# Kernel optimization log

Hardware: AMD Instinct MI355X
Metric: run time of the kernel (lower is better)

## Reference

```python
import jax, jax.numpy as jnp
import numpy as np

EPS = float(np.finfo(np.float32).eps)
H = 256          # hidden_size
K = 10           # num_event_types
B, S = 32, 4096  # batch, seq_len


def _linear_params(kw, kb, fan_in, fan_out):
    # torch nn.Linear default init (uniform +-1/sqrt(fan_in)), then abs + clamp(min=eps)
    bound = 1.0 / np.sqrt(fan_in)
    w = jnp.clip(jnp.abs(jax.random.uniform(kw, (fan_out, fan_in), minval=-bound, maxval=bound, dtype=jnp.float32)), EPS)
    b = jnp.clip(jnp.abs(jax.random.uniform(kb, (fan_out,), minval=-bound, maxval=bound, dtype=jnp.float32)), EPS)
    return w, b


def setup_inputs() -> dict:
    key = jax.random.key(0)
    ks = jax.random.split(key, 12)
    w1, b1 = _linear_params(ks[0], ks[1], 1, H)        # layer_dense_1
    w2, b2 = _linear_params(ks[2], ks[3], 2 * H, H)    # layer_dense_2
    wA, bA = _linear_params(ks[4], ks[5], H, H)        # module_list[0]
    wB, bB = _linear_params(ks[6], ks[7], H, H)        # module_list[1]
    w3, b3 = _linear_params(ks[8], ks[9], H, K)        # layer_dense_3 linear
    hidden_states = jax.random.normal(ks[10], (B, S, H), dtype=jnp.float32)
    time_delta_seqs = jax.random.uniform(ks[11], (B, S), dtype=jnp.float32)
    return dict(hidden_states=hidden_states, time_delta_seqs=time_delta_seqs,
                w1=w1, b1=b1, w2=w2, b2=b2, wA=wA, bA=bA, wB=wB, bB=bB, w3=w3, b3=b3)


def _cumul_hazard(td, h, w1, b1, w2, b2, wA, bA, wB, bB, w3, b3):
    # layer_dense_1: Linear(1 -> H) on td[..., None]
    t = td[..., None] * w1[:, 0] + b1                      # [B,S,H]
    out = jnp.tanh(jnp.concatenate([h, t], axis=-1) @ w2.T + b2)  # [B,S,H]
    out = jnp.tanh(out @ wA.T + bA)
    out = jnp.tanh(out @ wB.T + bB)
    return jax.nn.softplus(out @ w3.T + b3)                # [B,S,K]


def reference(hidden_states, time_delta_seqs, w1, b1, w2, b2, wA, bA, wB, bB, w3, b3):
    f = lambda td: _cumul_hazard(td, hidden_states, w1, b1, w2, b2, wA, bA, wB, bB, w3, b3)
    # Each output element depends only on its own t[b,s] (elementwise in time),
    # so a single forward-mode JVP with tangent=ones yields the exact per-element
    # derivative for ALL event types at once (fuses torch's per-type grad loop).
    integral_lambda, d_dt = jax.jvp(f, (time_delta_seqs,), (jnp.ones_like(time_delta_seqs),))
    # torch takes grad of .mean() over [B,S], which scales the derivative by 1/(B*S)
    derivative_integral_lambda = d_dt / time_delta_seqs.size
    return integral_lambda, derivative_integral_lambda
```

## Files before the change

### kernel.cpp

```cpp
#include <hip/hip_runtime.h>
#include <hip/hip_bf16.h>
#include <stdint.h>

typedef __bf16 bf16x8 __attribute__((ext_vector_type(8)));
typedef __bf16 bf16x4 __attribute__((ext_vector_type(4)));
typedef float  f32x4  __attribute__((ext_vector_type(4)));
typedef float  f32x2  __attribute__((ext_vector_type(2)));

#define MFMA16(a,b,c) __builtin_amdgcn_mfma_f32_16x16x32_bf16((a),(b),(c),0,0,0)

static constexpr int H_   = 256;
static constexpr int KEV  = 10;
static constexpr int NTOK = 32 * 4096;

__device__ __forceinline__ float ptanh(float x){
    float t = x * x;
    float n = fmaf(t, t + 105.0f, 945.0f);
    float d = fmaf(t, fmaf(t, 15.0f, 420.0f), 945.0f);
    float r = x * n * __builtin_amdgcn_rcpf(d);
    return __builtin_amdgcn_fmed3f(r, -1.0f, 1.0f);
}

__device__ __forceinline__ bf16x8 cvtFrag(const float* p){
    f32x4 a = *(const f32x4*)p;
    f32x4 b = *(const f32x4*)(p + 4);
    bf16x8 r;
    #pragma unroll
    for (int j = 0; j < 4; ++j){ r[j] = (__bf16)a[j]; r[4 + j] = (__bf16)b[j]; }
    return r;
}

__global__ void prep_vc(const float* __restrict__ w1, const float* __restrict__ b1,
                        const float* __restrict__ w2, const float* __restrict__ b2,
                        const float* __restrict__ b3, float* __restrict__ vc){
    int j = blockIdx.x * 4 + (threadIdx.x >> 6);
    int l = threadIdx.x & 63;
    const float* row = w2 + (size_t)j * (2 * H_) + H_;
    float v = 0.f, cc = 0.f;
    #pragma unroll
    for (int i = 0; i < 4; ++i){
        int k = l + 64 * i;
        float w = row[k];
        v  += w * w1[k];
        cc += w * b1[k];
    }
    #pragma unroll
    for (int off = 32; off; off >>= 1){
        v  += __shfl_down(v,  off, 64);
        cc += __shfl_down(cc, off, 64);
    }
    if (l == 0){ vc[j] = v; vc[H_ + j] = cc + b2[j]; }
    if (blockIdx.x == 0 && threadIdx.x < 16)
        vc[2 * H_ + threadIdx.x] = (threadIdx.x < KEV) ? b3[threadIdx.x] : 0.0f;
}

__global__ void prep_pack(const float* __restrict__ w2, const float* __restrict__ wA,
                          const float* __restrict__ wB, const float* __restrict__ w3,
                          __hip_bfloat16* __restrict__ pk){
    int b  = blockIdx.x;
    int L  = b >> 4, n0 = b & 15;
    const float* W; int K, nrows;
    if (b == 48){ W = w3; K = H_; nrows = KEV; }
    else { W = (L == 0) ? w2 : ((L == 1) ? wA : wB); K = (L == 0) ? 2 * H_ : H_; nrows = 16; }
    __hip_bfloat16* dst = pk + (size_t)b * 4096;
    int t = threadIdx.x;
    #pragma unroll
    for (int u = 0; u < 2; ++u){
        int slot = t * 2 + u;
        int s = slot >> 6, q = (slot >> 4) & 3, c = slot & 15;
        int rr = (b == 48) ? c : (n0 * 16 + c);
        if (c < nrows){
            const float* src = W + (size_t)rr * K + 32 * s + 8 * q;
            #pragma unroll
            for (int j = 0; j < 8; ++j) dst[slot * 8 + j] = __float2bfloat16(src[j]);
        } else {
            #pragma unroll
            for (int j = 0; j < 8; ++j) dst[slot * 8 + j] = __float2bfloat16(0.0f);
        }
    }
}

typedef const __attribute__((address_space(1))) void* gvp;
typedef __attribute__((address_space(3)))       void* lvp;

__device__ __forceinline__ void stage_chunk(const __hip_bfloat16* wpk, __hip_bfloat16* buf,
                                            int g, int wave, int lane){
    const char* src = (const char*)wpk + (size_t)g * 8192 + wave * 2048 + lane * 16;
    char*       dst = (char*)buf + wave * 2048;
    __builtin_amdgcn_global_load_lds((gvp)(const void*)src,          (lvp)(void*)dst,          16, 0, 0);
    __builtin_amdgcn_global_load_lds((gvp)(const void*)(src + 1024), (lvp)(void*)(dst + 1024), 16, 0, 0);
}

__global__ __launch_bounds__(256, 3) void chfn_kernel(
    const float* __restrict__ hs, const float* __restrict__ td,
    const __hip_bfloat16* __restrict__ wpk,
    const float* __restrict__ bA, const float* __restrict__ bB,
    const float* __restrict__ vc,
    float* __restrict__ out)
{
    __shared__ __hip_bfloat16 sW[2 * 4096];
    __shared__ __hip_bfloat16 sA[4 * 16 * H_];
    __shared__ __hip_bfloat16 sT[4 * 512];

    const int tid  = threadIdx.x;
    const int wave = tid >> 6;
    const int lane = tid & 63;
    const int q    = lane >> 4;
    const int c    = lane & 15;
    const int tb   = blockIdx.x * 64 + wave * 16;
    const int wrow = wave * 16;
    const int xr   = (c >> 1) & 7;
    const int sx   = (c >> 1) & 1;
    const int ws   = q * 16 + c;
    const int e0w  = wave * 512 + 32 * c + 4 * q;
    const int r0w  = wave * 512 + 32 * c + ((8 * q) ^ (sx << 4));

    stage_chunk(wpk, sW, 0, wave, lane);

    bf16x8 aF[8], TA[8], TB[8];
    {
        const float* h0 = hs + (size_t)(tb + c) * H_ + 8 * q;
        #pragma unroll
        for (int s = 0; s < 8; ++s) aF[s] = cvtFrag(h0 + 32 * s);
    }
    float myTd = td[tb + c];

    #pragma unroll
    for (int jj = 0; jj < 8; ++jj){
        #pragma unroll
        for (int t = 0; t < 2; ++t){
            int n0 = 2 * jj + t;
            __syncthreads();
            stage_chunk(wpk, sW + ((n0 + 1) & 1) * 4096, n0 + 1, wave, lane);
            bf16x8 W[8];
            {   const bf16x8* b = (const bf16x8*)(sW + (n0 & 1) * 4096) + ws;
                #pragma unroll
                for (int s = 0; s < 8; ++s) W[s] = b[s * 64];
            }
            f32x4 v4 = *(const f32x4*)(vc + n0 * 16 + 4 * q);
            f32x4 c4 = *(const f32x4*)(vc + H_ + n0 * 16 + 4 * q);
            f32x4 fa = c4;
            f32x4 fb = {0.f,0.f,0.f,0.f};
            #pragma unroll
            for (int s = 0; s < 4; ++s){
                fa = MFMA16(W[s],     aF[s],     fa);
                fb = MFMA16(W[s + 4], aF[s + 4], fb);
            }
            bf16x4 pa, pd;
            #pragma unroll
            for (int r = 0; r < 4; ++r){
                float x  = fmaf(myTd, v4[r], fa[r] + fb[r]);
                float th = ptanh(x);
                float dd = fmaf(-th, th, 1.0f) * v4[r];
                pa[r] = (__bf16)th; pd[r] = (__bf16)dd;
            }
            int chn = 2 * n0 + (q >> 1);
            int off = (wrow + c) * H_ + ((((chn + 4 * c) & 31) ^ xr) << 3) + ((q & 1) << 2);
            *(bf16x4*)((void*)(sA + off)) = pa;
            *(bf16x4*)((void*)(sT + e0w + ((t ^ sx) << 4))) = pd;
        }
        TB[jj] = *(const bf16x8*)(sT + r0w);
    }

    auto run_layer = [&](const float* __restrict__ bias, int g0,
                         bf16x8 (&Tin)[8], bf16x8 (&Tout)[8]){
        {
            const __hip_bfloat16* a0 = sA + (wrow + c) * H_;
            #pragma unroll
            for (int s = 0; s < 8; ++s){
                int g8 = ((((4 * s + q) + 4 * c) & 31) ^ xr) << 3;
                aF[s] = *(const bf16x8*)(a0 + g8);
            }
        }
        #pragma unroll
        for (int jj = 0; jj < 8; ++jj){
            #pragma unroll
            for (int t = 0; t < 2; ++t){
                int n0 = 2 * jj + t;
                int g  = g0 + n0;
                __syncthreads();
                stage_chunk(wpk, sW + ((g + 1) & 1) * 4096, g + 1, wave, lane);
                bf16x8 W[8];
                {   const bf16x8* b = (const bf16x8*)(sW + (g & 1) * 4096) + ws;
                    #pragma unroll
                    for (int s = 0; s < 8; ++s) W[s] = b[s * 64];
                }
                f32x4 b4 = *(const f32x4*)(bias + n0 * 16 + 4 * q);
                f32x4 fa = b4;
                f32x4 fb = {0.f,0.f,0.f,0.f};
                f32x4 ga = {0.f,0.f,0.f,0.f};
                f32x4 gb = {0.f,0.f,0.f,0.f};
                #pragma unroll
                for (int s = 0; s < 4; ++s){
                    fa = MFMA16(W[s],     aF[s],      fa);
                    ga = MFMA16(W[s],     Tin[s],     ga);
                    fb = MFMA16(W[s + 4], aF[s + 4],  fb);
                    gb = MFMA16(W[s + 4], Tin[s + 4], gb);
                }
                bf16x4 pa, pd;
                #pragma unroll
                for (int r = 0; r < 4; ++r){
                    float th = ptanh(fa[r] + fb[r]);
                    float dd = fmaf(-th, th, 1.0f) * (ga[r] + gb[r]);
                    pa[r] = (__bf16)th; pd[r] = (__bf16)dd;
                }
                int chn = 2 * n0 + (q >> 1);
                int off = (wrow + c) * H_ + ((((chn + 4 * c) & 31) ^ xr) << 3) + ((q & 1) << 2);
                *(bf16x4*)((void*)(sA + off)) = pa;
                *(bf16x4*)((void*)(sT + e0w + ((t ^ sx) << 4))) = pd;
            }
            Tout[jj] = *(const bf16x8*)(sT + r0w);
        }
    };

    run_layer(bA, 16, TB, TA);
    run_layer(bB, 32, TA, TB);

    {
        __syncthreads();
        bf16x8 W[8];
        {   const bf16x8* b = (const bf16x8*)sW + ws;
            #pragma unroll
            for (int s = 0; s < 8; ++s) W[s] = b[s * 64];
        }
        const __hip_bfloat16* a0 = sA + (wrow + c) * H_;
        #pragma unroll
        for (int s = 0; s < 8; ++s){
            int g8 = ((((4 * s + q) + 4 * c) & 31) ^ xr) << 3;
            aF[s] = *(const bf16x8*)(a0 + g8);
        }
        f32x4 b4 = *(const f32x4*)(vc + 2 * H_ + 4 * q);
        f32x4 fa = b4;
        f32x4 fb = {0.f,0.f,0.f,0.f};
        f32x4 ga = {0.f,0.f,0.f,0.f};
        f32x4 gb = {0.f,0.f,0.f,0.f};
        #pragma unroll
        for (int s = 0; s < 4; ++s){
            fa = MFMA16(W[s],     aF[s],     fa);
            ga = MFMA16(W[s],     TB[s],     ga);
            fb = MFMA16(W[s + 4], aF[s + 4], fb);
            gb = MFMA16(W[s + 4], TB[s + 4], gb);
        }
        int fbase = 4 * q;
        size_t token = tb + c;
        float sp[4], dv[4];
        #pragma unroll
        for (int r = 0; r < 4; ++r){
            float z  = fa[r] + fb[r];
            float a  = fabsf(z);
            float e  = __builtin_amdgcn_exp2f(-1.4426950408889634f * a);
            sp[r] = fmaxf(z, 0.f) + 0.69314718055994531f * __builtin_amdgcn_logf(1.0f + e);
            float sg = __builtin_amdgcn_rcpf(1.0f + e);
            sg = (z >= 0.f) ? sg : 1.0f - sg;
            dv[r] = sg * (ga[r] + gb[r]) * (1.0f / 131072.0f);
        }
        float* o0 = out + token * KEV + fbase;
        float* o1 = out + (size_t)NTOK * KEV + token * KEV + fbase;
        if (q < 2){
            *(f32x2*)o0       = (f32x2){sp[0], sp[1]};
            *(f32x2*)(o0 + 2) = (f32x2){sp[2], sp[3]};
            *(f32x2*)o1       = (f32x2){dv[0], dv[1]};
            *(f32x2*)(o1 + 2) = (f32x2){dv[2], dv[3]};
        } else if (q == 2){
            *(f32x2*)o0 = (f32x2){sp[0], sp[1]};
            *(f32x2*)o1 = (f32x2){dv[0], dv[1]};
        }
    }
}

extern "C" void kernel_launch(void* const* d_in, const int* in_sizes, int n_in,
                              void* d_out, int out_size, void* d_ws, size_t ws_size,
                              hipStream_t stream){
    const float* hs = (const float*)d_in[0];
    const float* td = (const float*)d_in[1];
    const float* w1 = (const float*)d_in[2];
    const float* b1 = (const float*)d_in[3];
    const float* w2 = (const float*)d_in[4];
    const float* b2 = (const float*)d_in[5];
    const float* wA = (const float*)d_in[6];
    const float* bA = (const float*)d_in[7];
    const float* wB = (const float*)d_in[8];
    const float* bB = (const float*)d_in[9];
    const float* w3 = (const float*)d_in[10];
    const float* b3 = (const float*)d_in[11];

    float*          vc  = (float*)d_ws;
    __hip_bfloat16* wpk = (__hip_bfloat16*)((char*)d_ws + 4096);
    float*          outp = (float*)d_out;

    prep_vc  <<<64, 256, 0, stream>>>(w1, b1, w2, b2, b3, vc);
    prep_pack<<<49, 256, 0, stream>>>(w2, wA, wB, w3, wpk);
    chfn_kernel<<<NTOK / 64, 256, 0, stream>>>(hs, td, wpk, bA, bB, vc, outp);
}
```

Measured before the change: 317.4 us.

## Split weight staging: half via LDS, half prefetched directly into registers

Each weight chunk is now split in two. One half is staged into LDS through global_load_lds as before. The other half is loaded straight from global memory into register double-buffers (Wg0/Wg1) one chunk ahead. This halves the LDS weight buffer and the LDS reads per chunk, which is meant to cut LDS traffic and footprint. In exchange it adds per-wave redundant global/L2 loads and more register pressure under launch_bounds(256,3), and latency exposure depends on the compiler placing waitcnts well.

Result: slower. 350.0 us (+10.3%).

```diff
diff --git a/kernel.cpp b/kernel.cpp
--- a/kernel.cpp
+++ b/kernel.cpp
@@ -83,12 +83,18 @@
 typedef const __attribute__((address_space(1))) void* gvp;
 typedef __attribute__((address_space(3)))       void* lvp;
 
-__device__ __forceinline__ void stage_chunk(const __hip_bfloat16* wpk, __hip_bfloat16* buf,
-                                            int g, int wave, int lane){
-    const char* src = (const char*)wpk + (size_t)g * 8192 + wave * 2048 + lane * 16;
-    char*       dst = (char*)buf + wave * 2048;
-    __builtin_amdgcn_global_load_lds((gvp)(const void*)src,          (lvp)(void*)dst,          16, 0, 0);
-    __builtin_amdgcn_global_load_lds((gvp)(const void*)(src + 1024), (lvp)(void*)(dst + 1024), 16, 0, 0);
+__device__ __forceinline__ void stage_half(const __hip_bfloat16* wpk, __hip_bfloat16* sW,
+                                           int g, int par, int wave, int lane){
+    const char* src = (const char*)wpk + (size_t)g * 8192 + wave * 1024 + lane * 16;
+    char*       dst = (char*)sW + par * 4096 + wave * 1024;
+    __builtin_amdgcn_global_load_lds((gvp)(const void*)src, (lvp)(void*)dst, 16, 0, 0);
+}
+
+__device__ __forceinline__ void pref_ghalf(const __hip_bfloat16* wpk, int g, int ws,
+                                           bf16x8 (&Wg)[4]){
+    const bf16x8* b = (const bf16x8*)((const char*)wpk + (size_t)g * 8192 + 4096);
+    #pragma unroll
+    for (int s = 0; s < 4; ++s) Wg[s] = b[s * 64 + ws];
 }
 
 __global__ __launch_bounds__(256, 3) void chfn_kernel(
@@ -98,7 +104,7 @@
     const float* __restrict__ vc,
     float* __restrict__ out)
 {
-    __shared__ __hip_bfloat16 sW[2 * 4096];
+    __shared__ __hip_bfloat16 sW[2 * 2048];
     __shared__ __hip_bfloat16 sA[4 * 16 * H_];
     __shared__ __hip_bfloat16 sT[4 * 512];
 
@@ -115,7 +121,10 @@
     const int e0w  = wave * 512 + 32 * c + 4 * q;
     const int r0w  = wave * 512 + 32 * c + ((8 * q) ^ (sx << 4));
 
-    stage_chunk(wpk, sW, 0, wave, lane);
+    bf16x8 Wg0[4], Wg1[4];
+
+    stage_half(wpk, sW, 0, 0, wave, lane);
+    pref_ghalf(wpk, 0, ws, Wg0);
 
     bf16x8 aF[8], TA[8], TB[8];
     {
@@ -131,20 +140,23 @@
         for (int t = 0; t < 2; ++t){
             int n0 = 2 * jj + t;
             __syncthreads();
-            stage_chunk(wpk, sW + ((n0 + 1) & 1) * 4096, n0 + 1, wave, lane);
-            bf16x8 W[8];
-            {   const bf16x8* b = (const bf16x8*)(sW + (n0 & 1) * 4096) + ws;
+            stage_half(wpk, sW, n0 + 1, (n0 + 1) & 1, wave, lane);
+            if (t == 0) pref_ghalf(wpk, n0 + 1, ws, Wg1);
+            else        pref_ghalf(wpk, n0 + 1, ws, Wg0);
+            bf16x8 Wl[4];
+            {   const bf16x8* bl = (const bf16x8*)((const char*)sW + (n0 & 1) * 4096);
                 #pragma unroll
-                for (int s = 0; s < 8; ++s) W[s] = b[s * 64];
-            }
+                for (int s = 0; s < 4; ++s) Wl[s] = bl[s * 64 + ws];
+            }
+            const bf16x8* Wgc = (t == 0) ? Wg0 : Wg1;
             f32x4 v4 = *(const f32x4*)(vc + n0 * 16 + 4 * q);
             f32x4 c4 = *(const f32x4*)(vc + H_ + n0 * 16 + 4 * q);
             f32x4 fa = c4;
             f32x4 fb = {0.f,0.f,0.f,0.f};
             #pragma unroll
             for (int s = 0; s < 4; ++s){
-                fa = MFMA16(W[s],     aF[s],     fa);
-                fb = MFMA16(W[s + 4], aF[s + 4], fb);
+                fa = MFMA16(Wl[s],  aF[s],     fa);
+                fb = MFMA16(Wgc[s], aF[s + 4], fb);
             }
             bf16x4 pa, pd;
             #pragma unroll
@@ -179,12 +191,15 @@
                 int n0 = 2 * jj + t;
                 int g  = g0 + n0;
                 __syncthreads();
-                stage_chunk(wpk, sW + ((g + 1) & 1) * 4096, g + 1, wave, lane);
-                bf16x8 W[8];
-                {   const bf16x8* b = (const bf16x8*)(sW + (g & 1) * 4096) + ws;
+                stage_half(wpk, sW, g + 1, (g + 1) & 1, wave, lane);
+                if (t == 0) pref_ghalf(wpk, g + 1, ws, Wg1);
+                else        pref_ghalf(wpk, g + 1, ws, Wg0);
+                bf16x8 Wl[4];
+                {   const bf16x8* bl = (const bf16x8*)((const char*)sW + (g & 1) * 4096);
                     #pragma unroll
-                    for (int s = 0; s < 8; ++s) W[s] = b[s * 64];
+                    for (int s = 0; s < 4; ++s) Wl[s] = bl[s * 64 + ws];
                 }
+                const bf16x8* Wgc = (t == 0) ? Wg0 : Wg1;
                 f32x4 b4 = *(const f32x4*)(bias + n0 * 16 + 4 * q);
                 f32x4 fa = b4;
                 f32x4 fb = {0.f,0.f,0.f,0.f};
@@ -192,10 +207,10 @@
                 f32x4 gb = {0.f,0.f,0.f,0.f};
                 #pragma unroll
                 for (int s = 0; s < 4; ++s){
-                    fa = MFMA16(W[s],     aF[s],      fa);
-                    ga = MFMA16(W[s],     Tin[s],     ga);
-                    fb = MFMA16(W[s + 4], aF[s + 4],  fb);
-                    gb = MFMA16(W[s + 4], Tin[s + 4], gb);
+                    fa = MFMA16(Wl[s],  aF[s],      fa);
+                    ga = MFMA16(Wl[s],  Tin[s],     ga);
+                    fb = MFMA16(Wgc[s], aF[s + 4],  fb);
+                    gb = MFMA16(Wgc[s], Tin[s + 4], gb);
                 }
                 bf16x4 pa, pd;
                 #pragma unroll
@@ -218,10 +233,10 @@
 
     {
         __syncthreads();
-        bf16x8 W[8];
-        {   const bf16x8* b = (const bf16x8*)sW + ws;
-            #pragma unroll
-            for (int s = 0; s < 8; ++s) W[s] = b[s * 64];
+        bf16x8 Wl[4];
+        {   const bf16x8* bl = (const bf16x8*)sW;
+            #pragma unroll
+            for (int s = 0; s < 4; ++s) Wl[s] = bl[s * 64 + ws];
         }
         const __hip_bfloat16* a0 = sA + (wrow + c) * H_;
         #pragma unroll
@@ -236,10 +251,10 @@
         f32x4 gb = {0.f,0.f,0.f,0.f};
         #pragma unroll
         for (int s = 0; s < 4; ++s){
-            fa = MFMA16(W[s],     aF[s],     fa);
-            ga = MFMA16(W[s],     TB[s],     ga);
-            fb = MFMA16(W[s + 4], aF[s + 4], fb);
-            gb = MFMA16(W[s + 4], TB[s + 4], gb);
+            fa = MFMA16(Wl[s],  aF[s],     fa);
+            ga = MFMA16(Wl[s],  TB[s],     ga);
+            fb = MFMA16(Wg0[s], aF[s + 4], fb);
+            gb = MFMA16(Wg0[s], TB[s + 4], gb);
         }
         int fbase = 4 * q;
         size_t token = tb + c;
```

## Stage weights in half-chunks through a three-slot LDS ring with explicit vmcnt waits

Applied to the files above, without the earlier changes.

Weight staging now moves half-chunks of 4 KB into a three-buffer LDS ring, always two halves ahead. Each step waits with an explicit `s_waitcnt vmcnt` and a raw `s_barrier` in place of a full `__syncthreads` per chunk. Each tile's MFMAs are split around the arrival of the second half, so compute on the first half can overlap the load of the next. Bias and vector constants are also preloaded into LDS once, so the per-tile loads no longer hit global memory. The cost is twice as many barriers, plus hand-written waitcnt logic that has to stay exactly right to avoid races.

Result: slower. 337.9 us (+6.5%).

```diff
diff --git a/kernel.cpp b/kernel.cpp
--- a/kernel.cpp
+++ b/kernel.cpp
@@ -83,12 +83,11 @@
 typedef const __attribute__((address_space(1))) void* gvp;
 typedef __attribute__((address_space(3)))       void* lvp;
 
-__device__ __forceinline__ void stage_chunk(const __hip_bfloat16* wpk, __hip_bfloat16* buf,
-                                            int g, int wave, int lane){
-    const char* src = (const char*)wpk + (size_t)g * 8192 + wave * 2048 + lane * 16;
-    char*       dst = (char*)buf + wave * 2048;
-    __builtin_amdgcn_global_load_lds((gvp)(const void*)src,          (lvp)(void*)dst,          16, 0, 0);
-    __builtin_amdgcn_global_load_lds((gvp)(const void*)(src + 1024), (lvp)(void*)(dst + 1024), 16, 0, 0);
+__device__ __forceinline__ void stage_half(const __hip_bfloat16* wpk, __hip_bfloat16* sW,
+                                           int h, int wave, int lane){
+    const char* src = (const char*)wpk + (size_t)h * 4096 + wave * 1024 + lane * 16;
+    char*       dst = (char*)sW + (h % 3) * 4096 + wave * 1024 + lane * 16;
+    __builtin_amdgcn_global_load_lds((gvp)(const void*)src, (lvp)(void*)dst, 16, 0, 0);
 }
 
 __global__ __launch_bounds__(256, 3) void chfn_kernel(
@@ -98,9 +97,10 @@
     const float* __restrict__ vc,
     float* __restrict__ out)
 {
-    __shared__ __hip_bfloat16 sW[2 * 4096];
+    __shared__ __hip_bfloat16 sW[3 * 2048];
     __shared__ __hip_bfloat16 sA[4 * 16 * H_];
     __shared__ __hip_bfloat16 sT[4 * 512];
+    __shared__ float          sB[1040];
 
     const int tid  = threadIdx.x;
     const int wave = tid >> 6;
@@ -115,8 +115,6 @@
     const int e0w  = wave * 512 + 32 * c + 4 * q;
     const int r0w  = wave * 512 + 32 * c + ((8 * q) ^ (sx << 4));
 
-    stage_chunk(wpk, sW, 0, wave, lane);
-
     bf16x8 aF[8], TA[8], TB[8];
     {
         const float* h0 = hs + (size_t)(tb + c) * H_ + 8 * q;
@@ -124,28 +122,44 @@
         for (int s = 0; s < 8; ++s) aF[s] = cvtFrag(h0 + 32 * s);
     }
     float myTd = td[tb + c];
+    for (int i = tid; i < 528; i += 256) sB[i] = vc[i];
+    sB[528 + tid] = bA[tid];
+    sB[784 + tid] = bB[tid];
+    __syncthreads();
+
+    stage_half(wpk, sW, 0, wave, lane);
+    stage_half(wpk, sW, 1, wave, lane);
+
+    auto phase = [&](int h){
+        if (h < 97) asm volatile("s_waitcnt vmcnt(1)" ::: "memory");
+        else        asm volatile("s_waitcnt vmcnt(0)" ::: "memory");
+        __builtin_amdgcn_s_barrier();
+        __builtin_amdgcn_sched_barrier(0);
+        if (h + 2 < 98) stage_half(wpk, sW, h + 2, wave, lane);
+    };
+    auto loadW = [&](int h, bf16x8 (&Wl)[4]){
+        const bf16x8* b = (const bf16x8*)(sW + (h % 3) * 2048);
+        #pragma unroll
+        for (int s = 0; s < 4; ++s) Wl[s] = b[s * 64 + ws];
+    };
 
     #pragma unroll
     for (int jj = 0; jj < 8; ++jj){
         #pragma unroll
         for (int t = 0; t < 2; ++t){
             int n0 = 2 * jj + t;
-            __syncthreads();
-            stage_chunk(wpk, sW + ((n0 + 1) & 1) * 4096, n0 + 1, wave, lane);
-            bf16x8 W[8];
-            {   const bf16x8* b = (const bf16x8*)(sW + (n0 & 1) * 4096) + ws;
-                #pragma unroll
-                for (int s = 0; s < 8; ++s) W[s] = b[s * 64];
-            }
-            f32x4 v4 = *(const f32x4*)(vc + n0 * 16 + 4 * q);
-            f32x4 c4 = *(const f32x4*)(vc + H_ + n0 * 16 + 4 * q);
+            int h  = 2 * n0;
+            bf16x8 W0[4], W1[4];
+            phase(h);     loadW(h, W0);
+            f32x4 v4 = *(const f32x4*)(sB + n0 * 16 + 4 * q);
+            f32x4 c4 = *(const f32x4*)(sB + 256 + n0 * 16 + 4 * q);
             f32x4 fa = c4;
             f32x4 fb = {0.f,0.f,0.f,0.f};
-            #pragma unroll
-            for (int s = 0; s < 4; ++s){
-                fa = MFMA16(W[s],     aF[s],     fa);
-                fb = MFMA16(W[s + 4], aF[s + 4], fb);
-            }
+            fa = MFMA16(W0[0], aF[0], fa); fb = MFMA16(W0[1], aF[1], fb);
+            fa = MFMA16(W0[2], aF[2], fa); fb = MFMA16(W0[3], aF[3], fb);
+            phase(h + 1); loadW(h + 1, W1);
+            fa = MFMA16(W1[0], aF[4], fa); fb = MFMA16(W1[1], aF[5], fb);
+            fa = MFMA16(W1[2], aF[6], fa); fb = MFMA16(W1[3], aF[7], fb);
             bf16x4 pa, pd;
             #pragma unroll
             for (int r = 0; r < 4; ++r){
@@ -177,26 +191,23 @@
             #pragma unroll
             for (int t = 0; t < 2; ++t){
                 int n0 = 2 * jj + t;
-                int g  = g0 + n0;
-                __syncthreads();
-                stage_chunk(wpk, sW + ((g + 1) & 1) * 4096, g + 1, wave, lane);
-                bf16x8 W[8];
-                {   const bf16x8* b = (const bf16x8*)(sW + (g & 1) * 4096) + ws;
-                    #pragma unroll
-                    for (int s = 0; s < 8; ++s) W[s] = b[s * 64];
-                }
+                int h  = 2 * (g0 + n0);
+                bf16x8 W0[4], W1[4];
+                phase(h);     loadW(h, W0);
                 f32x4 b4 = *(const f32x4*)(bias + n0 * 16 + 4 * q);
                 f32x4 fa = b4;
                 f32x4 fb = {0.f,0.f,0.f,0.f};
                 f32x4 ga = {0.f,0.f,0.f,0.f};
                 f32x4 gb = {0.f,0.f,0.f,0.f};
-                #pragma unroll
-                for (int s = 0; s < 4; ++s){
-                    fa = MFMA16(W[s],     aF[s],      fa);
-                    ga = MFMA16(W[s],     Tin[s],     ga);
-                    fb = MFMA16(W[s + 4], aF[s + 4],  fb);
-                    gb = MFMA16(W[s + 4], Tin[s + 4], gb);
-                }
+                fa = MFMA16(W0[0], aF[0],  fa); ga = MFMA16(W0[0], Tin[0],  ga);
+                fb = MFMA16(W0[1], aF[1],  fb); gb = MFMA16(W0[1], Tin[1],  gb);
+                fa = MFMA16(W0[2], aF[2],  fa); ga = MFMA16(W0[2], Tin[2],  ga);
+                fb = MFMA16(W0[3], aF[3],  fb); gb = MFMA16(W0[3], Tin[3],  gb);
+                phase(h + 1); loadW(h + 1, W1);
+                fa = MFMA16(W1[0], aF[4],  fa); ga = MFMA16(W1[0], Tin[4],  ga);
+                fb = MFMA16(W1[1], aF[5],  fb); gb = MFMA16(W1[1], Tin[5],  gb);
+                fa = MFMA16(W1[2], aF[6],  fa); ga = MFMA16(W1[2], Tin[6],  ga);
+                fb = MFMA16(W1[3], aF[7],  fb); gb = MFMA16(W1[3], Tin[7],  gb);
                 bf16x4 pa, pd;
                 #pragma unroll
                 for (int r = 0; r < 4; ++r){
@@ -213,34 +224,32 @@
         }
     };
 
-    run_layer(bA, 16, TB, TA);
-    run_layer(bB, 32, TA, TB);
+    run_layer(sB + 528, 16, TB, TA);
+    run_layer(sB + 784, 32, TA, TB);
 
     {
-        __syncthreads();
-        bf16x8 W[8];
-        {   const bf16x8* b = (const bf16x8*)sW + ws;
-            #pragma unroll
-            for (int s = 0; s < 8; ++s) W[s] = b[s * 64];
-        }
+        bf16x8 W0[4], W1[4];
         const __hip_bfloat16* a0 = sA + (wrow + c) * H_;
         #pragma unroll
         for (int s = 0; s < 8; ++s){
             int g8 = ((((4 * s + q) + 4 * c) & 31) ^ xr) << 3;
             aF[s] = *(const bf16x8*)(a0 + g8);
         }
-        f32x4 b4 = *(const f32x4*)(vc + 2 * H_ + 4 * q);
+        f32x4 b4 = *(const f32x4*)(sB + 512 + 4 * q);
         f32x4 fa = b4;
         f32x4 fb = {0.f,0.f,0.f,0.f};
         f32x4 ga = {0.f,0.f,0.f,0.f};
         f32x4 gb = {0.f,0.f,0.f,0.f};
-        #pragma unroll
-        for (int s = 0; s < 4; ++s){
-            fa = MFMA16(W[s],     aF[s],     fa);
-            ga = MFMA16(W[s],     TB[s],     ga);
-            fb = MFMA16(W[s + 4], aF[s + 4], fb);
-            gb = MFMA16(W[s + 4], TB[s + 4], gb);
-        }
+        phase(96); loadW(96, W0);
+        fa = MFMA16(W0[0], aF[0], fa); ga = MFMA16(W0[0], TB[0], ga);
+        fb = MFMA16(W0[1], aF[1], fb); gb = MFMA16(W0[1], TB[1], gb);
+        fa = MFMA16(W0[2], aF[2], fa); ga = MFMA16(W0[2], TB[2], ga);
+        fb = MFMA16(W0[3], aF[3], fb); gb = MFMA16(W0[3], TB[3], gb);
+        phase(97); loadW(97, W1);
+        fa = MFMA16(W1[0], aF[4], fa); ga = MFMA16(W1[0], TB[4], ga);
+        fb = MFMA16(W1[1], aF[5], fb); gb = MFMA16(W1[1], TB[5], gb);
+        fa = MFMA16(W1[2], aF[6], fa); ga = MFMA16(W1[2], TB[6], ga);
+        fb = MFMA16(W1[3], aF[7], fb); gb = MFMA16(W1[3], TB[7], gb);
         int fbase = 4 * q;
         size_t token = tb + c;
         float sp[4], dv[4];
```
